# Kernel optimization log

Hardware: AMD Instinct MI355X
Metric: run time of the kernel (lower is better)

Reference implementation:

```python
import jax, jax.numpy as jnp
import numpy as np

EPS = 1e-5

def rmsnorm(x):
    # BitLinear pre-norm (no learnable scale), per BitNet b1.58 reference impl
    return x * jax.lax.rsqrt(jnp.mean(x * x, axis=-1, keepdims=True) + EPS)

def act_quant(x):
    # per-token absmax 8-bit quantization with straight-through estimator
    scale = 127.0 / jnp.clip(jnp.max(jnp.abs(x), axis=-1, keepdims=True), 1e-5)
    q = jnp.clip(jnp.round(x * scale), -128.0, 127.0) / scale
    return x + jax.lax.stop_gradient(q - x)

def weight_quant(w):
    # absmean ternary quantization {-1,0,1} with STE
    scale = 1.0 / jnp.clip(jnp.mean(jnp.abs(w)), 1e-5)
    q = jnp.clip(jnp.round(w * scale), -1.0, 1.0) / scale
    return w + jax.lax.stop_gradient(q - w)

def bitlinear(x, w, b):
    # x: [b, s, d_in], w: [d_out, d_in] (torch Linear layout), b: [d_out]
    xq = act_quant(rmsnorm(x))
    wq = weight_quant(w)
    return jnp.einsum('bsd,fd->bsf', xq, wq) + b

def setup_inputs() -> dict:
    key = jax.random.key(0)
    k0, k1, k2 = jax.random.split(key, 3)
    B, S, D, F = 2, 8192, 1024, 4096  # inner_dim = dim * mult = 4096
    x = jax.random.normal(k0, (B, S, D), dtype=jnp.float32)
    w1 = jax.random.normal(k1, (F, D), dtype=jnp.float32) * (1.0 / np.sqrt(D))
    b1 = jnp.zeros((F,), dtype=jnp.float32)
    w2 = jax.random.normal(k2, (D, F), dtype=jnp.float32) * (1.0 / np.sqrt(F))
    b2 = jnp.zeros((D,), dtype=jnp.float32)
    return {"x": x, "w1": w1, "b1": b1, "w2": w2, "b2": b2}

def reference(x, w1, b1, w2, b2):
    h = bitlinear(x, w1, b1)
    h = jax.nn.gelu(h, approximate=False)  # nn.GELU() default is exact
    # post_act_ln=False -> no LayerNorm; dropout p=0.0 -> identity
    return bitlinear(h, w2, b2)
```

## Files before the change

kernel.cpp:

```cpp
#include <hip/hip_runtime.h>
#include <hip/hip_bf16.h>
#include <stdint.h>

typedef int i32x4 __attribute__((ext_vector_type(4)));

__device__ __forceinline__ float blo(unsigned int u) {
  unsigned int v = u << 16; float f; __builtin_memcpy(&f, &v, 4); return f;
}
__device__ __forceinline__ float bhi(unsigned int u) {
  unsigned int v = u & 0xffff0000u; float f; __builtin_memcpy(&f, &v, 4); return f;
}
__device__ __forceinline__ int pack4q(float a, float b, float c, float d, float qm) {
  int i0 = (int)rintf(a * qm) & 255;
  int i1 = (int)rintf(b * qm) & 255;
  int i2 = (int)rintf(c * qm) & 255;
  int i3 = (int)rintf(d * qm) & 255;
  return i0 | (i1 << 8) | (i2 << 16) | (i3 << 24);
}

__device__ __forceinline__ float fast_gelu(float v) {
  float u = v * 0.70710678118654752f;
  float s = fabsf(u);
  float den = fmaf(0.3275911f, s, 1.0f);
  float t;
  asm("v_rcp_f32 %0, %1" : "=v"(t) : "v"(den));
  float p = t * fmaf(t, fmaf(t, fmaf(t, fmaf(t, 1.061405429f, -1.453152027f),
                                     1.421413741f), -0.284496736f), 0.254829592f);
  float e = fmaf(-p, __expf(-u * u), 1.0f);
  float er = copysignf(e, u);
  return 0.5f * v * (1.0f + er);
}

__global__ void k_reduce_abs(const float* __restrict__ w, long n4, float* __restrict__ partials) {
  const float4* wv = (const float4*)w;
  float s = 0.0f;
  long stride = (long)gridDim.x * blockDim.x;
  for (long i = (long)blockIdx.x * blockDim.x + threadIdx.x; i < n4; i += stride) {
    float4 v = wv[i];
    s += fabsf(v.x) + fabsf(v.y) + fabsf(v.z) + fabsf(v.w);
  }
  #pragma unroll
  for (int off = 32; off; off >>= 1) s += __shfl_down(s, off);
  __shared__ float sw[4];
  if ((threadIdx.x & 63) == 0) sw[threadIdx.x >> 6] = s;
  __syncthreads();
  if (threadIdx.x == 0) partials[blockIdx.x] = sw[0] + sw[1] + sw[2] + sw[3];
}

__global__ void k_finalize_scales(const float* __restrict__ p1, const float* __restrict__ p2,
                                  float* __restrict__ scales, float inv1, float inv2) {
  int t = threadIdx.x;
  float s1 = p1[t], s2 = p2[t];
  #pragma unroll
  for (int off = 32; off; off >>= 1) { s1 += __shfl_down(s1, off); s2 += __shfl_down(s2, off); }
  __shared__ float a1[4], a2[4];
  if ((t & 63) == 0) { a1[t >> 6] = s1; a2[t >> 6] = s2; }
  __syncthreads();
  if (t == 0) {
    scales[0] = fmaxf((a1[0]+a1[1]+a1[2]+a1[3]) * inv1, 1e-5f);
    scales[1] = fmaxf((a2[0]+a2[1]+a2[2]+a2[3]) * inv2, 1e-5f);
  }
}

__global__ void k_quant_w(const float* __restrict__ w, char* __restrict__ wq,
                          long n4, const float* __restrict__ scales, int which) {
  float s = 1.0f / scales[which];
  const float4* wv = (const float4*)w;
  int* qv = (int*)wq;
  long stride = (long)gridDim.x * blockDim.x;
  for (long i = (long)blockIdx.x * blockDim.x + threadIdx.x; i < n4; i += stride) {
    float4 v = wv[i];
    int b0 = (int)fminf(fmaxf(rintf(v.x * s), -1.0f), 1.0f) & 255;
    int b1 = (int)fminf(fmaxf(rintf(v.y * s), -1.0f), 1.0f) & 255;
    int b2 = (int)fminf(fmaxf(rintf(v.z * s), -1.0f), 1.0f) & 255;
    int b3 = (int)fminf(fmaxf(rintf(v.w * s), -1.0f), 1.0f) & 255;
    qv[i] = b0 | (b1 << 8) | (b2 << 16) | (b3 << 24);
  }
}

__global__ void k_actq_x(const float* __restrict__ x, char* __restrict__ xq,
                         float* __restrict__ alpha) {
  const int D = 1024;
  size_t t = blockIdx.x;
  int tid = threadIdx.x;
  const float4* row = (const float4*)(x + t * (size_t)D);
  float4 v = row[tid];
  float ss = v.x*v.x + v.y*v.y + v.z*v.z + v.w*v.w;
  float am = fmaxf(fmaxf(fabsf(v.x), fabsf(v.y)), fmaxf(fabsf(v.z), fabsf(v.w)));
  #pragma unroll
  for (int off = 32; off; off >>= 1) {
    ss += __shfl_down(ss, off);
    am = fmaxf(am, __shfl_down(am, off));
  }
  __shared__ float s_ss[4], s_am[4];
  if ((tid & 63) == 0) { s_ss[tid >> 6] = ss; s_am[tid >> 6] = am; }
  __syncthreads();
  ss = s_ss[0] + s_ss[1] + s_ss[2] + s_ss[3];
  am = fmaxf(fmaxf(s_am[0], s_am[1]), fmaxf(s_am[2], s_am[3]));
  float rms = rsqrtf(ss * (1.0f / D) + 1e-5f);
  float a   = fmaxf(am * rms, 1e-5f);
  float qs  = 127.0f / a;
  if (tid == 0) alpha[t] = a * (1.0f / 127.0f);
  int b0 = (int)fminf(fmaxf(rintf((v.x * rms) * qs), -128.0f), 127.0f) & 255;
  int b1 = (int)fminf(fmaxf(rintf((v.y * rms) * qs), -128.0f), 127.0f) & 255;
  int b2 = (int)fminf(fmaxf(rintf((v.z * rms) * qs), -128.0f), 127.0f) & 255;
  int b3 = (int)fminf(fmaxf(rintf((v.w * rms) * qs), -128.0f), 127.0f) & 255;
  ((int*)xq)[t * 256 + tid] = b0 | (b1 << 8) | (b2 << 16) | (b3 << 24);
}

__global__ void k_actq_h(__hip_bfloat16* __restrict__ h, float* __restrict__ alpha) {
  const int F = 4096;
  size_t t = blockIdx.x;
  int tid = threadIdx.x;
  char* rb = (char*)(h + t * (size_t)F);
  const uint4* row = (const uint4*)rb;
  uint4 u0 = row[tid], u1 = row[tid + 256];
  unsigned int uu[8] = {u0.x, u0.y, u0.z, u0.w, u1.x, u1.y, u1.z, u1.w};
  float ss = 0.0f, am = 0.0f;
  #pragma unroll
  for (int i = 0; i < 8; i++) {
    float f0 = blo(uu[i]), f1 = bhi(uu[i]);
    ss += f0 * f0 + f1 * f1;
    am = fmaxf(am, fmaxf(fabsf(f0), fabsf(f1)));
  }
  #pragma unroll
  for (int off = 32; off; off >>= 1) {
    ss += __shfl_down(ss, off);
    am = fmaxf(am, __shfl_down(am, off));
  }
  __shared__ float s_ss[4], s_am[4];
  if ((tid & 63) == 0) { s_ss[tid >> 6] = ss; s_am[tid >> 6] = am; }
  __syncthreads();
  ss = s_ss[0] + s_ss[1] + s_ss[2] + s_ss[3];
  am = fmaxf(fmaxf(s_am[0], s_am[1]), fmaxf(s_am[2], s_am[3]));
  float rms = rsqrtf(ss * (1.0f / F) + 1e-5f);
  float a   = fmaxf(am * rms, 1e-5f);
  float qm  = rms * (127.0f / a);
  if (tid == 0) alpha[t] = a * (1.0f / 127.0f);
  uint2 w0, w1;
  w0.x = (unsigned)pack4q(blo(uu[0]), bhi(uu[0]), blo(uu[1]), bhi(uu[1]), qm);
  w0.y = (unsigned)pack4q(blo(uu[2]), bhi(uu[2]), blo(uu[3]), bhi(uu[3]), qm);
  w1.x = (unsigned)pack4q(blo(uu[4]), bhi(uu[4]), blo(uu[5]), bhi(uu[5]), qm);
  w1.y = (unsigned)pack4q(blo(uu[6]), bhi(uu[6]), blo(uu[7]), bhi(uu[7]), qm);
  *(uint2*)(rb + 8 * tid) = w0;
  *(uint2*)(rb + 2048 + 8 * tid) = w1;
}

#define GLD16(GP, LP) __builtin_amdgcn_global_load_lds( \
    (__attribute__((address_space(1))) void*)(GP), \
    (__attribute__((address_space(3))) void*)(LP), 16, 0, 0)
#define VMCNT0 asm volatile("s_waitcnt vmcnt(0)" ::: "memory")
#define LGKM0  do { asm volatile("s_waitcnt lgkmcnt(0)" ::: "memory"); __builtin_amdgcn_sched_barrier(0); } while(0)

template<int EPI>
__global__ __launch_bounds__(512, 4) void k_gemm_i8(
    const char* __restrict__ A, int lda,
    const char* __restrict__ B,
    const float* __restrict__ bias, const float* __restrict__ alpha,
    const float* __restrict__ scales, int which,
    void* __restrict__ Cout, int N, int K, int lgnbx)
{
  __shared__ __align__(16) char lA[2 * 8192];
  __shared__ __align__(16) char lB[2 * 16384];
  const int tid = threadIdx.x, lane = tid & 63, wid = tid >> 6;
  const int wm = wid >> 2, wn = wid & 3;
  const int nwg = gridDim.x, bid = blockIdx.x;
  const int swz = (bid & 7) * (nwg >> 3) + (bid >> 3);
  const int bx = swz & ((1 << lgnbx) - 1), by = swz >> lgnbx;
  const int m0 = by * 128, n0 = bx * 256;
  const int NT = K >> 6;

  const int srow = tid >> 2, slot = tid & 3;
  const int sswz = (slot ^ ((srow >> 1) & 3)) * 16;
  const char* gA0 = A + (size_t)(m0 +       srow) * lda + sswz;
  const char* gB0 = B + (size_t)(n0 +       srow) * K   + sswz;
  const char* gB1 = B + (size_t)(n0 + 128 + srow) * K   + sswz;
  const int ldst = srow * 64 + slot * 16;

  const int lr = lane & 15;
  const int kx = ((lane >> 4) ^ ((lane >> 1) & 3)) * 16;
  const int aoff = (wm * 64 + lr) * 64 + kx;
  const int boff = (wn * 64 + lr) * 64 + kx;

  GLD16(gA0, lA + ldst);
  GLD16(gB0, lB + ldst);
  GLD16(gB1, lB + 8192 + ldst);

  i32x4 acc[4][4] = {};
  for (int t = 0; t < NT; ++t) {
    const int cur = t & 1, nxt = cur ^ 1;
    VMCNT0;
    __builtin_amdgcn_s_barrier();
    if (t + 1 < NT) {
      GLD16(gA0 + 64 * (t + 1), lA + nxt * 8192 + ldst);
      GLD16(gB0 + 64 * (t + 1), lB + nxt * 16384 + ldst);
      GLD16(gB1 + 64 * (t + 1), lB + nxt * 16384 + 8192 + ldst);
    }
    i32x4 av[4], bv[4];
    {
      const char* pa = lA + cur * 8192 + aoff;
      const char* pb = lB + cur * 16384 + boff;
      #pragma unroll
      for (int j = 0; j < 4; ++j) av[j] = *(const i32x4*)(pa + j * 1024);
      #pragma unroll
      for (int n = 0; n < 4; ++n) bv[n] = *(const i32x4*)(pb + n * 1024);
    }
    LGKM0;
    __builtin_amdgcn_s_setprio(1);
    #pragma unroll
    for (int j = 0; j < 4; ++j)
      #pragma unroll
      for (int n = 0; n < 4; ++n)
        acc[j][n] = __builtin_amdgcn_mfma_i32_16x16x64_i8(av[j], bv[n], acc[j][n], 0, 0, 0);
    __builtin_amdgcn_s_setprio(0);
  }

  const float wdq = scales[which];
  const int lq4 = (lane >> 4) * 4;
  #pragma unroll
  for (int m = 0; m < 4; ++m) {
    const int rowb = m0 + wm * 64 + m * 16 + lq4;
    float al[4];
    #pragma unroll
    for (int q = 0; q < 4; ++q) al[q] = alpha[rowb + q] * wdq;
    #pragma unroll
    for (int n = 0; n < 4; ++n) {
      const int col = n0 + wn * 64 + n * 16 + lr;
      const float bb = bias[col];
      #pragma unroll
      for (int q = 0; q < 4; ++q) {
        float v = (float)acc[m][n][q] * al[q] + bb;
        if constexpr (EPI == 0) {
          ((__hip_bfloat16*)Cout)[(size_t)(rowb + q) * N + col] = __float2bfloat16(fast_gelu(v));
        } else {
          ((float*)Cout)[(size_t)(rowb + q) * N + col] = v;
        }
      }
    }
  }
}

extern "C" void kernel_launch(void* const* d_in, const int* in_sizes, int n_in,
                              void* d_out, int out_size, void* d_ws, size_t ws_size,
                              hipStream_t stream) {
  const float* x  = (const float*)d_in[0];
  const float* w1 = (const float*)d_in[1];
  const float* b1 = (const float*)d_in[2];
  const float* w2 = (const float*)d_in[3];
  const float* b2 = (const float*)d_in[4];
  const int  F = in_sizes[2];
  const int  D = in_sizes[4];
  const long T = (long)in_sizes[0] / D;
  const long nW = (long)F * D;

  char* ws = (char*)d_ws;
  float* partials1 = (float*)ws;
  float* partials2 = partials1 + 256;
  float* scales    = partials2 + 256;
  float* alpha1 = (float*)(ws + 4096);
  float* alpha2 = alpha1 + T;
  size_t off = 4096 + 2 * (size_t)T * sizeof(float);
  off = (off + 255) & ~(size_t)255;
  char* w1q = ws + off; off += (size_t)nW;
  char* w2q = ws + off; off += (size_t)nW;
  char* xq  = ws + off; off += (size_t)T * D;
  off = (off + 255) & ~(size_t)255;
  __hip_bfloat16* h = (__hip_bfloat16*)(ws + off); off += (size_t)T * F * 2;
  if (ws_size < off) return;

  float invW = (float)(1.0 / (double)nW);
  k_reduce_abs<<<256, 256, 0, stream>>>(w1, nW / 4, partials1);
  k_reduce_abs<<<256, 256, 0, stream>>>(w2, nW / 4, partials2);
  k_finalize_scales<<<1, 256, 0, stream>>>(partials1, partials2, scales, invW, invW);
  k_quant_w<<<2048, 256, 0, stream>>>(w1, w1q, nW / 4, scales, 0);
  k_quant_w<<<2048, 256, 0, stream>>>(w2, w2q, nW / 4, scales, 1);
  k_actq_x<<<(unsigned)T, 256, 0, stream>>>(x, xq, alpha1);

  dim3 g1((unsigned)((T / 128) * (F / 256)));
  k_gemm_i8<0><<<g1, 512, 0, stream>>>(xq, D, w1q, b1, alpha1, scales, 0,
                                       h, F, D, __builtin_ctz(F / 256));

  k_actq_h<<<(unsigned)T, 256, 0, stream>>>(h, alpha2);

  dim3 g2((unsigned)((T / 128) * (D / 256)));
  k_gemm_i8<1><<<g2, 512, 0, stream>>>((const char*)h, F * 2, w2q, b2, alpha2, scales, 1,
                                       (float*)d_out, D, F, __builtin_ctz(D / 256));
}
```

Measured before the change: 257.9 us.

## Triple-buffer int8 GEMM LDS pipeline and merge weight prep kernels

The int8 GEMM now keeps three LDS stages and prefetches two k-tiles ahead, waiting with vmcnt(3) so one stage of global loads stays in flight during the MFMAs. Separately, the per-weight abs-reduction and ternary quantization kernels are each merged into one launch covering both weight matrices. This targets exposed global-load latency in the GEMM main loop and launch overhead in weight preparation. The larger LDS footprint (72KB per block) may reduce blocks resident per CU.

Result: faster. 244.4 us (-5.2%).

```diff
diff --git a/kernel.cpp b/kernel.cpp
--- a/kernel.cpp
+++ b/kernel.cpp
@@ -31,11 +31,15 @@
   return 0.5f * v * (1.0f + er);
 }
 
-__global__ void k_reduce_abs(const float* __restrict__ w, long n4, float* __restrict__ partials) {
+__global__ void k_reduce_abs2(const float* __restrict__ w1, const float* __restrict__ w2,
+                              long n4, float* __restrict__ partials) {
+  const int half = gridDim.x >> 1;
+  const float* w = (blockIdx.x < half) ? w1 : w2;
+  int b = (blockIdx.x < half) ? blockIdx.x : blockIdx.x - half;
   const float4* wv = (const float4*)w;
   float s = 0.0f;
-  long stride = (long)gridDim.x * blockDim.x;
-  for (long i = (long)blockIdx.x * blockDim.x + threadIdx.x; i < n4; i += stride) {
+  long stride = (long)half * blockDim.x;
+  for (long i = (long)b * blockDim.x + threadIdx.x; i < n4; i += stride) {
     float4 v = wv[i];
     s += fabsf(v.x) + fabsf(v.y) + fabsf(v.z) + fabsf(v.w);
   }
@@ -62,13 +66,19 @@
   }
 }
 
-__global__ void k_quant_w(const float* __restrict__ w, char* __restrict__ wq,
-                          long n4, const float* __restrict__ scales, int which) {
-  float s = 1.0f / scales[which];
+__global__ void k_quant_w2(const float* __restrict__ w1, char* __restrict__ wq1,
+                           const float* __restrict__ w2, char* __restrict__ wq2,
+                           long n4, const float* __restrict__ scales) {
+  const int half = gridDim.x >> 1;
+  const bool first = blockIdx.x < half;
+  const float* w = first ? w1 : w2;
+  char* wq = first ? wq1 : wq2;
+  int b = first ? blockIdx.x : blockIdx.x - half;
+  float s = 1.0f / scales[first ? 0 : 1];
   const float4* wv = (const float4*)w;
   int* qv = (int*)wq;
-  long stride = (long)gridDim.x * blockDim.x;
-  for (long i = (long)blockIdx.x * blockDim.x + threadIdx.x; i < n4; i += stride) {
+  long stride = (long)half * blockDim.x;
+  for (long i = (long)b * blockDim.x + threadIdx.x; i < n4; i += stride) {
     float4 v = wv[i];
     int b0 = (int)fminf(fmaxf(rintf(v.x * s), -1.0f), 1.0f) & 255;
     int b1 = (int)fminf(fmaxf(rintf(v.y * s), -1.0f), 1.0f) & 255;
@@ -149,6 +159,7 @@
 #define GLD16(GP, LP) __builtin_amdgcn_global_load_lds( \
     (__attribute__((address_space(1))) void*)(GP), \
     (__attribute__((address_space(3))) void*)(LP), 16, 0, 0)
+#define VMCNT3 asm volatile("s_waitcnt vmcnt(3)" ::: "memory")
 #define VMCNT0 asm volatile("s_waitcnt vmcnt(0)" ::: "memory")
 #define LGKM0  do { asm volatile("s_waitcnt lgkmcnt(0)" ::: "memory"); __builtin_amdgcn_sched_barrier(0); } while(0)
 
@@ -160,8 +171,8 @@
     const float* __restrict__ scales, int which,
     void* __restrict__ Cout, int N, int K, int lgnbx)
 {
-  __shared__ __align__(16) char lA[2 * 8192];
-  __shared__ __align__(16) char lB[2 * 16384];
+  __shared__ __align__(16) char lA[3 * 8192];
+  __shared__ __align__(16) char lB[3 * 16384];
   const int tid = threadIdx.x, lane = tid & 63, wid = tid >> 6;
   const int wm = wid >> 2, wn = wid & 3;
   const int nwg = gridDim.x, bid = blockIdx.x;
@@ -182,19 +193,22 @@
   const int aoff = (wm * 64 + lr) * 64 + kx;
   const int boff = (wn * 64 + lr) * 64 + kx;
 
-  GLD16(gA0, lA + ldst);
-  GLD16(gB0, lB + ldst);
-  GLD16(gB1, lB + 8192 + ldst);
+  GLD16(gA0,      lA + ldst);
+  GLD16(gB0,      lB + ldst);
+  GLD16(gB1,      lB + 8192 + ldst);
+  GLD16(gA0 + 64, lA + 8192 + ldst);
+  GLD16(gB0 + 64, lB + 16384 + ldst);
+  GLD16(gB1 + 64, lB + 16384 + 8192 + ldst);
 
   i32x4 acc[4][4] = {};
+  int cur = 0, nx1 = 1, nx2 = 2;
   for (int t = 0; t < NT; ++t) {
-    const int cur = t & 1, nxt = cur ^ 1;
-    VMCNT0;
+    if (t + 1 < NT) { VMCNT3; } else { VMCNT0; }
     __builtin_amdgcn_s_barrier();
-    if (t + 1 < NT) {
-      GLD16(gA0 + 64 * (t + 1), lA + nxt * 8192 + ldst);
-      GLD16(gB0 + 64 * (t + 1), lB + nxt * 16384 + ldst);
-      GLD16(gB1 + 64 * (t + 1), lB + nxt * 16384 + 8192 + ldst);
+    if (t + 2 < NT) {
+      GLD16(gA0 + 64 * (t + 2), lA + nx2 * 8192 + ldst);
+      GLD16(gB0 + 64 * (t + 2), lB + nx2 * 16384 + ldst);
+      GLD16(gB1 + 64 * (t + 2), lB + nx2 * 16384 + 8192 + ldst);
     }
     i32x4 av[4], bv[4];
     {
@@ -213,6 +227,7 @@
       for (int n = 0; n < 4; ++n)
         acc[j][n] = __builtin_amdgcn_mfma_i32_16x16x64_i8(av[j], bv[n], acc[j][n], 0, 0, 0);
     __builtin_amdgcn_s_setprio(0);
+    int tmp = cur; cur = nx1; nx1 = nx2; nx2 = tmp;
   }
 
   const float wdq = scales[which];
@@ -254,9 +269,8 @@
   const long nW = (long)F * D;
 
   char* ws = (char*)d_ws;
-  float* partials1 = (float*)ws;
-  float* partials2 = partials1 + 256;
-  float* scales    = partials2 + 256;
+  float* partials = (float*)ws;
+  float* scales   = partials + 512;
   float* alpha1 = (float*)(ws + 4096);
   float* alpha2 = alpha1 + T;
   size_t off = 4096 + 2 * (size_t)T * sizeof(float);
@@ -269,11 +283,9 @@
   if (ws_size < off) return;
 
   float invW = (float)(1.0 / (double)nW);
-  k_reduce_abs<<<256, 256, 0, stream>>>(w1, nW / 4, partials1);
-  k_reduce_abs<<<256, 256, 0, stream>>>(w2, nW / 4, partials2);
-  k_finalize_scales<<<1, 256, 0, stream>>>(partials1, partials2, scales, invW, invW);
-  k_quant_w<<<2048, 256, 0, stream>>>(w1, w1q, nW / 4, scales, 0);
-  k_quant_w<<<2048, 256, 0, stream>>>(w2, w2q, nW / 4, scales, 1);
+  k_reduce_abs2<<<512, 256, 0, stream>>>(w1, w2, nW / 4, partials);
+  k_finalize_scales<<<1, 256, 0, stream>>>(partials, partials + 256, scales, invW, invW);
+  k_quant_w2<<<4096, 256, 0, stream>>>(w1, w1q, w2, w2q, nW / 4, scales);
   k_actq_x<<<(unsigned)T, 256, 0, stream>>>(x, xq, alpha1);
 
   dim3 g1((unsigned)((T / 128) * (F / 256)));
```
